# Kernel optimization log

Hardware: AMD Instinct MI355X
Metric: run time of the kernel (lower is better)

## Reference

```python
import jax, jax.numpy as jnp
import numpy as np

NC = 10          # num_clusters
D_MODEL = 512
H = 8
DK = 64          # d_model = H*DK
B = 8
L = 2048


def _mlp2(x, W1, b1, W2, b2):
    h = jax.nn.gelu(x @ W1 + b1, approximate=False)
    return h @ W2 + b2


def setup_inputs() -> dict:
    key = jax.random.key(0)
    ks = jax.random.split(key, 12)
    s_in = 1.0 / np.sqrt(D_MODEL)
    s_h = 1.0 / np.sqrt(4 * NC)
    s_nc = 1.0 / np.sqrt(NC)
    return {
        "Q": jax.random.normal(ks[0], (B, H, L, DK), jnp.float32),
        "K": jax.random.normal(ks[1], (B, H, L, DK), jnp.float32),
        "V": jax.random.normal(ks[2], (B, H, L, DK), jnp.float32),
        # cluster_k_proj: Linear(d_model,4*nc) GELU Linear(4*nc,nc); stored as [in,out]
        "Wk1": jax.random.normal(ks[3], (D_MODEL, 4 * NC), jnp.float32) * s_in,
        "bk1": jnp.zeros((4 * NC,), jnp.float32),
        "Wk2": jax.random.normal(ks[4], (4 * NC, NC), jnp.float32) * s_h,
        "bk2": jnp.zeros((NC,), jnp.float32),
        # cluster_q_proj
        "Wq1": jax.random.normal(ks[5], (D_MODEL, 4 * NC), jnp.float32) * s_in,
        "bq1": jnp.zeros((4 * NC,), jnp.float32),
        "Wq2": jax.random.normal(ks[6], (4 * NC, NC), jnp.float32) * s_h,
        "bq2": jnp.zeros((NC,), jnp.float32),
        # proj_back_to_cluster_k: Linear(nc, d_model) + GELU
        "Wp": jax.random.normal(ks[7], (NC, D_MODEL), jnp.float32) * s_nc,
        "bp": jnp.zeros((D_MODEL,), jnp.float32),
    }


def _forward(Q, K, V, Wk1, bk1, Wk2, bk2, Wq1, bq1, Wq2, bq2, Wp, bp):
    b, h, l, d_k = Q.shape
    nc = Wk2.shape[1]
    unfolding = 10 * nc

    def pool(x):
        # torch: MaxPool1d(kernel=9, stride=9(default), padding=4) on reshape(b, d_k*h, -1)
        x3 = x.reshape(b, d_k * h, -1)
        y = jax.lax.reduce_window(x3, -jnp.inf, jax.lax.max,
                                  (1, 1, 9), (1, 1, 9),
                                  ((0, 0), (0, 0), (4, 4)))
        return y.reshape(b, h, -1, d_k)

    Kp = pool(K)
    Vp = pool(V)
    l_k = Kp.shape[2]

    # pad along batch dim and take sliding windows of size `unfolding` (stride 1)
    pad = jnp.zeros((unfolding, h, l_k, d_k), Kp.dtype)
    K_padded = jnp.concatenate([pad, Kp[1:]], axis=0)      # [unfolding+b-1, h, l_k, d_k]
    idx = jnp.arange(b)[:, None] + jnp.arange(unfolding)[None, :]
    K_unf = K_padded[idx]                                  # [b, unfolding, h, l_k, d_k]
    K_unf = jnp.transpose(K_unf, (0, 2, 3, 4, 1))          # torch unfold puts window last
    K_unf = K_unf.reshape(b, l_k, unfolding, d_k * h)      # row-major reshape, as torch

    ck = jax.nn.softmax(_mlp2(K_unf, Wk1, bk1, Wk2, bk2), axis=-1)  # [b,l_k,u,nc]
    cq = jax.nn.softmax(_mlp2(K_unf, Wq1, bq1, Wq2, bq2), axis=-1)

    mu = jnp.mean(cq, axis=-1)                             # [b, l_k, unfolding]
    sigma = jax.nn.softplus(jnp.std(cq, axis=-1, ddof=1))  # torch std is unbiased
    x = jnp.mean(ck, axis=-1)
    log_prob = -0.5 * jnp.square((x - mu) / sigma) - jnp.log(sigma) - 0.5 * jnp.log(2.0 * jnp.pi)
    # torch CrossEntropyLoss(mu, mu): classes are dim 1 (l_k), soft prob targets
    logp = jax.nn.log_softmax(mu, axis=1)
    ce = jnp.mean(-jnp.sum(mu * logp, axis=1))
    loss = -jnp.mean(log_prob) + ce

    # fused scatter-style cluster centers: mean over window of cq with assigned cluster zeroed
    assign = jnp.argmax(cq, axis=-1)                       # [b, l_k, unfolding]
    onehot = jax.nn.one_hot(assign, nc, dtype=cq.dtype)    # [b, l_k, u, i] (constant wrt grad)
    total = jnp.sum(cq, axis=2)                            # [b, l_k, nc]
    S = jnp.einsum('blui,bluc->blic', onehot, cq)          # sum of cq at masked positions
    centers = (total[:, :, None, :] - S) / unfolding       # [b, l_k, nc_i, nc_c]
    centers = jnp.transpose(centers, (2, 0, 1, 3))         # [nc, b, l_k, nc]

    cc = jax.nn.gelu(centers @ Wp + bp, approximate=False) # [nc, b, l_k, d_model]
    cc = cc.reshape(b, h, nc, l_k, d_k)                    # faithful torch reshape

    scores = jnp.einsum('bhqd,bhckd->bhqk', Q, cc) / np.sqrt(d_k).astype(Q.dtype)
    attn = jax.nn.softmax(scores, axis=-1)
    context = jnp.einsum('bhqk,bhkd->bhqd', attn, Vp)
    return context, loss


def reference(Q, K, V, Wk1, bk1, Wk2, bk2, Wq1, bq1, Wq2, bq2, Wp, bp):
    return _forward(Q, K, V, Wk1, bk1, Wk2, bk2, Wq1, bq1, Wq2, bq2, Wp, bp)
```

## Files before the change

kernel.cpp:

```cpp
#include <hip/hip_runtime.h>
#include <math.h>

#define NCL 10
#define DM 512
#define NH 8
#define DK 64
#define NB 8
#define SL 2048
#define LK 228
#define UF 100
#define KP_PER_B (NH*LK*DK)
#define KP_TOT (NB*KP_PER_B)
#define NROWS (NB*LK*UF)
#define POOL_BLOCKS 7296

typedef __bf16 bf16_t;
typedef __attribute__((ext_vector_type(2))) __bf16 bf16x2;
typedef __attribute__((ext_vector_type(8))) __bf16 bf16x8;
typedef __attribute__((ext_vector_type(4))) float f32x4;

__device__ __forceinline__ float gelu_f(float x) {
    return 0.5f * x * (1.f + erff(x * 0.70710678118654752f));
}

__global__ void k_pool(const float* __restrict__ K, const float* __restrict__ V,
                       float* __restrict__ Kp, float* __restrict__ Vp,
                       const float* __restrict__ Wq1, bf16_t* __restrict__ W1b,
                       float* __restrict__ acc) {
    int bid = blockIdx.x;
    if (bid >= POOL_BLOCKS) {
        int i = (bid - POOL_BLOCKS) * 256 + threadIdx.x;
        if (i < 512 * 40) W1b[i] = (bf16_t)Wq1[i];
        if (bid == POOL_BLOCKS && threadIdx.x < 4) acc[threadIdx.x] = 0.f;
        return;
    }
    int idx = bid * 256 + threadIdx.x;
    const float* src = (idx < KP_TOT) ? K : V;
    float* dst = (idx < KP_TOT) ? Kp : Vp;
    int e = (idx < KP_TOT) ? idx : idx - KP_TOT;
    int b   = e / KP_PER_B;
    int off = e % KP_PER_B;
    int c  = off / LK;
    int pp = off % LK;
    int p0 = pp * 9 - 4;
    const float* base = src + (size_t)b * 1048576 + (size_t)c * 2048;
    float mx = -3.4e38f;
    #pragma unroll
    for (int j = 0; j < 9; ++j) {
        int p = p0 + j;
        if (p >= 0 && p < 2048) mx = fmaxf(mx, base[p]);
    }
    dst[e] = mx;
}

template<int B>
__device__ __forceinline__ void layer1(int tid, const bf16_t* __restrict__ W1b,
                                       const float* __restrict__ Sstf,
                                       float* __restrict__ hT) {
    #pragma unroll 1
    for (int k = 0; k < 2; ++k) {
        int vt = tid + (k << 8);
        if (vt < 500) {
            int m = vt / 5;
            int h8 = vt - m * 5;
            int bm = (12 * m) % 100;
            float h[8];
            #pragma unroll
            for (int i = 0; i < 8; ++i) h[i] = 0.f;
            #pragma unroll
            for (int s = 1; s <= B; ++s) {
                const int t = 99 - B + s;
                int d0 = t - bm; if (d0 < 0) d0 += 100;
                int r0 = ((m << 9) + d0 - t) / 100;
                const float* srow = &Sstf[s << 9];
                #pragma unroll
                for (int j = 0; j < 6; ++j) {
                    int c = d0 + j * 100;
                    if (j < 5 || c < 512) {
                        float v = srow[r0 + j];
                        bf16x8 w = *(const bf16x8*)&W1b[c * 40 + h8 * 8];
                        #pragma unroll
                        for (int i = 0; i < 8; ++i)
                            h[i] = fmaf(v, (float)w[i], h[i]);
                    }
                }
            }
            #pragma unroll
            for (int i = 0; i < 8; ++i) hT[m * 44 + h8 * 8 + i] = h[i];
        }
    }
}

__global__ __launch_bounds__(256, 4) void k_mlp(
        const float* __restrict__ Kp, const bf16_t* __restrict__ W1b,
        const float* __restrict__ bq1,
        const float* __restrict__ Wq2, const float* __restrict__ bq2,
        float* __restrict__ mu_g, float* __restrict__ centers_g,
        float* __restrict__ acc_g) {
    __shared__ __align__(16) char smem[34432];
    float* Sstf  = (float*)smem;
    float* hT    = (float*)(smem + 16384);
    float* stats = (float*)(smem + 33984);

    int tid = threadIdx.x;
    int bl = blockIdx.x;
    int b = bl / LK;
    int l = bl % LK;

    for (int s4 = tid; s4 < 128 * b; s4 += 256) {
        int bk = (s4 >> 7) + 1;
        int r4 = (s4 & 127) << 2;
        *(float4*)&Sstf[(bk << 9) + r4] =
            *(const float4*)&Kp[bk * KP_PER_B + l * 512 + r4];
    }
    if (tid < 111) stats[tid] = 0.f;
    if (b == 0) {
        for (int i = tid; i < 4400; i += 256) hT[i] = 0.f;
    }
    __syncthreads();

    switch (b) {
        case 1: layer1<1>(tid, W1b, Sstf, hT); break;
        case 2: layer1<2>(tid, W1b, Sstf, hT); break;
        case 3: layer1<3>(tid, W1b, Sstf, hT); break;
        case 4: layer1<4>(tid, W1b, Sstf, hT); break;
        case 5: layer1<5>(tid, W1b, Sstf, hT); break;
        case 6: layer1<6>(tid, W1b, Sstf, hT); break;
        case 7: layer1<7>(tid, W1b, Sstf, hT); break;
        default: break;
    }
    __syncthreads();

    for (int i = tid; i < 4000; i += 256) {
        int row = i / 40;
        int j = i - row * 40;
        hT[row * 44 + j] = gelu_f(hT[row * 44 + j] + bq1[j]);
    }
    __syncthreads();

    float* total_l = stats;
    float* S_l = stats + 10;
    float* lp_acc = stats + 110;

    if (tid < 100) {
        int row = tid;
        float g[40];
        #pragma unroll
        for (int j4 = 0; j4 < 10; ++j4) {
            float4 gv = *(const float4*)&hT[row * 44 + j4 * 4];
            g[j4 * 4 + 0] = gv.x; g[j4 * 4 + 1] = gv.y;
            g[j4 * 4 + 2] = gv.z; g[j4 * 4 + 3] = gv.w;
        }
        float out[10];
        #pragma unroll
        for (int c = 0; c < 10; ++c) out[c] = bq2[c];
        #pragma unroll
        for (int j = 0; j < 40; ++j) {
            float gj = g[j];
            #pragma unroll
            for (int c = 0; c < 10; ++c)
                out[c] = fmaf(gj, Wq2[j * 10 + c], out[c]);
        }
        float m = out[0]; int am = 0;
        #pragma unroll
        for (int c = 1; c < 10; ++c)
            if (out[c] > m) { m = out[c]; am = c; }
        float e[10], s = 0.f;
        #pragma unroll
        for (int c = 0; c < 10; ++c) { e[c] = expf(out[c] - m); s += e[c]; }
        float inv = 1.f / s;
        float cq[10], s1 = 0.f;
        #pragma unroll
        for (int c = 0; c < 10; ++c) { cq[c] = e[c] * inv; s1 += cq[c]; }
        float mean = s1 * 0.1f;
        float var = 0.f;
        #pragma unroll
        for (int c = 0; c < 10; ++c) { float d = cq[c] - mean; var += d * d; }
        float sd = sqrtf(var / 9.f);
        float sp = log1pf(expf(sd));
        float lp = -logf(sp) - 0.91893853320467274f;
        mu_g[bl * 100 + row] = mean;
        atomicAdd(lp_acc, lp);
        #pragma unroll
        for (int c = 0; c < 10; ++c) {
            atomicAdd(&total_l[c], cq[c]);
            atomicAdd(&S_l[am * 10 + c], cq[c]);
        }
    }
    __syncthreads();
    if (tid == 0) atomicAdd(&acc_g[0], lp_acc[0]);
    if (tid < 100) {
        centers_g[bl * 100 + tid] = (total_l[tid % 10] - S_l[tid]) * 0.01f;
    }
}

__global__ void k_ce(const float* __restrict__ mu_g, float* __restrict__ acc_g,
                     float* __restrict__ outp) {
    int bid = blockIdx.x;
    int b = bid / 100;
    int u = bid % 100;
    int lane = threadIdx.x;
    float v[4];
    #pragma unroll
    for (int t = 0; t < 4; ++t) {
        int l = lane + t * 64;
        v[t] = (l < LK) ? mu_g[(b * LK + l) * 100 + u] : -3.4e38f;
    }
    float m = fmaxf(fmaxf(v[0], v[1]), fmaxf(v[2], v[3]));
    for (int o = 32; o > 0; o >>= 1) m = fmaxf(m, __shfl_xor(m, o, 64));
    float se = 0.f;
    #pragma unroll
    for (int t = 0; t < 4; ++t) {
        int l = lane + t * 64;
        if (l < LK) se += expf(v[t] - m);
    }
    for (int o = 32; o > 0; o >>= 1) se += __shfl_xor(se, o, 64);
    float lse = m + logf(se);
    float dot = 0.f;
    #pragma unroll
    for (int t = 0; t < 4; ++t) {
        int l = lane + t * 64;
        if (l < LK) dot += v[t] * (v[t] - lse);
    }
    for (int o = 32; o > 0; o >>= 1) dot += __shfl_xor(dot, o, 64);
    if (lane == 0) {
        atomicAdd(&acc_g[1], -dot * (1.f / 800.f));
        __threadfence();
        unsigned int old = atomicAdd((unsigned int*)&acc_g[2], 1u);
        if (old == 799u) {
            __threadfence();
            outp[8388608] = -(acc_g[0] * (1.f / (float)NROWS)) + acc_g[1];
        }
    }
}

__global__ void k_ccs(const float* __restrict__ centers_g,
                      const float* __restrict__ Wp, const float* __restrict__ bp,
                      float* __restrict__ ccs) {
    int tid = blockIdx.x * 256 + threadIdx.x;
    if (tid >= KP_TOT) return;
    int k2d2 = tid % (LK * DK);
    int bh = tid / (LK * DK);
    float s = 0.f;
    #pragma unroll
    for (int i2 = 0; i2 < 10; ++i2) {
        int t2 = bh * 145920 + i2 * 14592 + k2d2;
        int i = t2 / 933888;
        int r1 = t2 % 933888;
        int bs = r1 / 116736;
        int r2 = r1 % 116736;
        int ls = r2 / 512;
        int mm = r2 % 512;
        const float* cen = centers_g + (bs * LK + ls) * 100 + i * 10;
        float val = bp[mm];
        #pragma unroll
        for (int c = 0; c < 10; ++c)
            val = fmaf(cen[c], Wp[c * 512 + mm], val);
        s += gelu_f(val);
    }
    ccs[tid] = s;
}

#define QT 128
__global__ __launch_bounds__(256, 3) void k_attn(
        const float* __restrict__ Q, const float* __restrict__ ccs,
        const float* __restrict__ Vp, float* __restrict__ outp) {
    __shared__ __align__(16) char smem[36864];
    bf16_t* Kl = (bf16_t*)(smem);
    bf16_t* Vt = (bf16_t*)(smem + 9216);
    bf16_t* Pl = (bf16_t*)(smem + 18432);

    int tid = threadIdx.x;
    int wid = tid >> 6;
    int lane = tid & 63;
    int ln = lane & 15;
    int qd = lane >> 4;
    int bid = blockIdx.x;
    int bh = bid >> 4;
    int qt = bid & 15;
    int qbase = qt * QT;

    const float* Qbh = Q + (size_t)bh * SL * DK;
    const float* Kbh = ccs + (size_t)bh * LK * DK;
    const float* Vbh = Vp + (size_t)bh * LK * DK;

    for (int s = tid; s < QT * 32; s += 256) {
        int r = s >> 5;
        int c2 = s & 31;
        float2 v = *(const float2*)&Qbh[(size_t)(qbase + r) * DK + c2 * 2];
        *(bf16x2*)&Pl[r * 72 + c2 * 2] = (bf16x2){(bf16_t)v.x, (bf16_t)v.y};
    }
    __syncthreads();
    bf16x8 qf[2][2];
    #pragma unroll
    for (int mt = 0; mt < 2; ++mt)
        #pragma unroll
        for (int ks = 0; ks < 2; ++ks)
            qf[mt][ks] = *(const bf16x8*)&Pl[(wid * 32 + mt * 16 + ln) * 72 + ks * 32 + qd * 8];

    f32x4 acc_o[2][4];
    float mrow[2][4], lrow[2][4];
    #pragma unroll
    for (int mt = 0; mt < 2; ++mt)
        #pragma unroll
        for (int t = 0; t < 4; ++t) {
            acc_o[mt][t] = (f32x4)(0.f);
            mrow[mt][t] = -3.0e38f;
            lrow[mt][t] = 0.f;
        }

    for (int ch = 0; ch < 4; ++ch) {
        int k0 = ch * 64;
        __syncthreads();
        for (int s = tid; s < 64 * 32; s += 256) {
            int kk = s >> 5;
            int c2 = s & 31;
            int key = k0 + kk;
            float2 v = (key < LK) ? *(const float2*)&Kbh[(size_t)key * DK + c2 * 2]
                                  : make_float2(0.f, 0.f);
            *(bf16x2*)&Kl[kk * 72 + c2 * 2] = (bf16x2){(bf16_t)v.x, (bf16_t)v.y};
        }
        for (int s = tid; s < 64 * 16; s += 256) {
            int kk = s >> 4;
            int c4 = s & 15;
            int key = k0 + kk;
            float4 v = (key < LK) ? *(const float4*)&Vbh[(size_t)key * DK + c4 * 4]
                                  : make_float4(0.f, 0.f, 0.f, 0.f);
            Vt[(c4 * 4 + 0) * 72 + kk] = (bf16_t)v.x;
            Vt[(c4 * 4 + 1) * 72 + kk] = (bf16_t)v.y;
            Vt[(c4 * 4 + 2) * 72 + kk] = (bf16_t)v.z;
            Vt[(c4 * 4 + 3) * 72 + kk] = (bf16_t)v.w;
        }
        __syncthreads();

        f32x4 accs[2][4];
        #pragma unroll
        for (int mt = 0; mt < 2; ++mt)
            #pragma unroll
            for (int nt = 0; nt < 4; ++nt) accs[mt][nt] = (f32x4)(0.f);
        #pragma unroll
        for (int ks = 0; ks < 2; ++ks) {
            #pragma unroll
            for (int nt = 0; nt < 4; ++nt) {
                bf16x8 bf = *(const bf16x8*)&Kl[(nt * 16 + ln) * 72 + ks * 32 + qd * 8];
                #pragma unroll
                for (int mt = 0; mt < 2; ++mt)
                    accs[mt][nt] = __builtin_amdgcn_mfma_f32_16x16x32_bf16(qf[mt][ks], bf, accs[mt][nt], 0, 0, 0);
            }
        }

        #pragma unroll
        for (int mt = 0; mt < 2; ++mt) {
            #pragma unroll
            for (int r = 0; r < 4; ++r) {
                float sv[4];
                #pragma unroll
                for (int nt = 0; nt < 4; ++nt) {
                    float s = accs[mt][nt][r] * 0.125f;
                    int key = k0 + nt * 16 + ln;
                    sv[nt] = (key < LK) ? s : -3.0e38f;
                }
                float rmax = fmaxf(fmaxf(sv[0], sv[1]), fmaxf(sv[2], sv[3]));
                #pragma unroll
                for (int o = 1; o < 16; o <<= 1)
                    rmax = fmaxf(rmax, __shfl_xor(rmax, o, 64));
                float mold = mrow[mt][r];
                float mnew = fmaxf(mold, rmax);
                float alpha = __expf(mold - mnew);
                float p[4], psum = 0.f;
                #pragma unroll
                for (int nt = 0; nt < 4; ++nt) {
                    p[nt] = __expf(sv[nt] - mnew);
                    psum += p[nt];
                }
                #pragma unroll
                for (int o = 1; o < 16; o <<= 1)
                    psum += __shfl_xor(psum, o, 64);
                lrow[mt][r] = lrow[mt][r] * alpha + psum;
                mrow[mt][r] = mnew;
                #pragma unroll
                for (int ntv = 0; ntv < 4; ++ntv)
                    acc_o[mt][ntv][r] *= alpha;
                int prow = (wid * 32 + mt * 16 + qd * 4 + r) * 72;
                #pragma unroll
                for (int nt = 0; nt < 4; ++nt)
                    Pl[prow + nt * 16 + ln] = (bf16_t)p[nt];
            }
        }

        #pragma unroll
        for (int ks = 0; ks < 2; ++ks) {
            bf16x8 pa[2];
            #pragma unroll
            for (int mt = 0; mt < 2; ++mt)
                pa[mt] = *(const bf16x8*)&Pl[(wid * 32 + mt * 16 + ln) * 72 + ks * 32 + qd * 8];
            #pragma unroll
            for (int ntv = 0; ntv < 4; ++ntv) {
                bf16x8 vb = *(const bf16x8*)&Vt[(ntv * 16 + ln) * 72 + ks * 32 + qd * 8];
                #pragma unroll
                for (int mt = 0; mt < 2; ++mt)
                    acc_o[mt][ntv] = __builtin_amdgcn_mfma_f32_16x16x32_bf16(pa[mt], vb, acc_o[mt][ntv], 0, 0, 0);
            }
        }
    }

    #pragma unroll
    for (int mt = 0; mt < 2; ++mt) {
        #pragma unroll
        for (int r = 0; r < 4; ++r) {
            float inv = 1.f / lrow[mt][r];
            int q_idx = qbase + wid * 32 + mt * 16 + qd * 4 + r;
            float* orow = outp + ((size_t)bh * SL + q_idx) * DK;
            #pragma unroll
            for (int ntv = 0; ntv < 4; ++ntv)
                orow[ntv * 16 + ln] = acc_o[mt][ntv][r] * inv;
        }
    }
}

extern "C" void kernel_launch(void* const* d_in, const int* in_sizes, int n_in,
                              void* d_out, int out_size, void* d_ws, size_t ws_size,
                              hipStream_t stream) {
    const float* Q   = (const float*)d_in[0];
    const float* K   = (const float*)d_in[1];
    const float* V   = (const float*)d_in[2];
    const float* Wq1 = (const float*)d_in[7];
    const float* bq1 = (const float*)d_in[8];
    const float* Wq2 = (const float*)d_in[9];
    const float* bq2 = (const float*)d_in[10];
    const float* Wp  = (const float*)d_in[11];
    const float* bp  = (const float*)d_in[12];
    float* out = (float*)d_out;

    float* ws      = (float*)d_ws;
    float* Kp      = ws;
    float* Vp      = ws + 933888;
    float* mu      = ws + 1867776;
    float* centers = ws + 2050176;
    float* ccs     = ws + 2232576;
    float* acc     = ws + 3166464;
    bf16_t* W1b    = (bf16_t*)(ws + 3166468);

    k_pool<<<POOL_BLOCKS + 80, 256, 0, stream>>>(K, V, Kp, Vp, Wq1, W1b, acc);
    k_mlp<<<NB * LK, 256, 0, stream>>>(Kp, W1b, bq1, Wq2, bq2, mu, centers, acc);
    k_ccs<<<(KP_TOT + 255) / 256, 256, 0, stream>>>(centers, Wp, bp, ccs);
    k_ce<<<NB * 100, 64, 0, stream>>>(mu, acc, out);
    k_attn<<<NB * NH * (SL / QT), 256, 0, stream>>>(Q, ccs, Vp, out);
}
```

Baseline: 349.8 us.

## Fuse GELU and second MLP layer into layer1, shrink shared memory

Folds the GELU and the second linear layer into the first-layer loop. Each thread's 8 hidden outputs are immediately multiplied by Wq2 and accumulated into a 100x10 shared buffer with atomics, so the 100x44 hidden staging buffer, one barrier and a separate GELU pass go away. Shared memory shrinks (Sstf drops its unused b=0 slot), launch bounds rise to 8 blocks per CU, and the block index is remapped so that consecutive blocks take different batches, which interleaves light and heavy work. The cost is shared-memory atomic contention (five threads per row) and extra register pressure from the fused epilogue.

```diff
diff --git a/kernel.cpp b/kernel.cpp
--- a/kernel.cpp
+++ b/kernel.cpp
@@ -56,7 +56,9 @@
 template<int B>
 __device__ __forceinline__ void layer1(int tid, const bf16_t* __restrict__ W1b,
                                        const float* __restrict__ Sstf,
-                                       float* __restrict__ hT) {
+                                       const float* __restrict__ bq1,
+                                       const float* __restrict__ Wq2,
+                                       float* __restrict__ pout) {
     #pragma unroll 1
     for (int k = 0; k < 2; ++k) {
         int vt = tid + (k << 8);
@@ -72,7 +74,7 @@
                 const int t = 99 - B + s;
                 int d0 = t - bm; if (d0 < 0) d0 += 100;
                 int r0 = ((m << 9) + d0 - t) / 100;
-                const float* srow = &Sstf[s << 9];
+                const float* srow = &Sstf[(s - 1) << 9];
                 #pragma unroll
                 for (int j = 0; j < 6; ++j) {
                     int c = d0 + j * 100;
@@ -85,56 +87,62 @@
                     }
                 }
             }
-            #pragma unroll
-            for (int i = 0; i < 8; ++i) hT[m * 44 + h8 * 8 + i] = h[i];
-        }
-    }
-}
-
-__global__ __launch_bounds__(256, 4) void k_mlp(
+            float po[10];
+            #pragma unroll
+            for (int c = 0; c < 10; ++c) po[c] = 0.f;
+            #pragma unroll
+            for (int i = 0; i < 8; ++i) {
+                float g = gelu_f(h[i] + bq1[h8 * 8 + i]);
+                const float* w2row = &Wq2[(h8 * 8 + i) * 10];
+                #pragma unroll
+                for (int c = 0; c < 10; ++c)
+                    po[c] = fmaf(g, w2row[c], po[c]);
+            }
+            #pragma unroll
+            for (int c = 0; c < 10; ++c)
+                atomicAdd(&pout[m * 10 + c], po[c]);
+        }
+    }
+}
+
+__global__ __launch_bounds__(256, 8) void k_mlp(
         const float* __restrict__ Kp, const bf16_t* __restrict__ W1b,
         const float* __restrict__ bq1,
         const float* __restrict__ Wq2, const float* __restrict__ bq2,
         float* __restrict__ mu_g, float* __restrict__ centers_g,
         float* __restrict__ acc_g) {
-    __shared__ __align__(16) char smem[34432];
+    __shared__ __align__(16) char smem[18784];
     float* Sstf  = (float*)smem;
-    float* hT    = (float*)(smem + 16384);
-    float* stats = (float*)(smem + 33984);
+    float* pout  = (float*)(smem + 14336);
+    float* stats = (float*)(smem + 18336);
 
     int tid = threadIdx.x;
-    int bl = blockIdx.x;
-    int b = bl / LK;
-    int l = bl % LK;
+    int bid = blockIdx.x;
+    int b = bid & 7;
+    int l = bid >> 3;
+    int bl = b * LK + l;
 
     for (int s4 = tid; s4 < 128 * b; s4 += 256) {
         int bk = (s4 >> 7) + 1;
         int r4 = (s4 & 127) << 2;
-        *(float4*)&Sstf[(bk << 9) + r4] =
+        *(float4*)&Sstf[((bk - 1) << 9) + r4] =
             *(const float4*)&Kp[bk * KP_PER_B + l * 512 + r4];
     }
+    if (b > 0) {
+        for (int i = tid; i < 1000; i += 256) pout[i] = 0.f;
+    }
     if (tid < 111) stats[tid] = 0.f;
-    if (b == 0) {
-        for (int i = tid; i < 4400; i += 256) hT[i] = 0.f;
-    }
     __syncthreads();
 
     switch (b) {
-        case 1: layer1<1>(tid, W1b, Sstf, hT); break;
-        case 2: layer1<2>(tid, W1b, Sstf, hT); break;
-        case 3: layer1<3>(tid, W1b, Sstf, hT); break;
-        case 4: layer1<4>(tid, W1b, Sstf, hT); break;
-        case 5: layer1<5>(tid, W1b, Sstf, hT); break;
-        case 6: layer1<6>(tid, W1b, Sstf, hT); break;
-        case 7: layer1<7>(tid, W1b, Sstf, hT); break;
+        case 1: layer1<1>(tid, W1b, Sstf, bq1, Wq2, pout); break;
+        case 2: layer1<2>(tid, W1b, Sstf, bq1, Wq2, pout); break;
+        case 3: layer1<3>(tid, W1b, Sstf, bq1, Wq2, pout); break;
+        case 4: layer1<4>(tid, W1b, Sstf, bq1, Wq2, pout); break;
+        case 5: layer1<5>(tid, W1b, Sstf, bq1, Wq2, pout); break;
+        case 6: layer1<6>(tid, W1b, Sstf, bq1, Wq2, pout); break;
+        case 7: layer1<7>(tid, W1b, Sstf, bq1, Wq2, pout); break;
         default: break;
-    }
-    __syncthreads();
-
-    for (int i = tid; i < 4000; i += 256) {
-        int row = i / 40;
-        int j = i - row * 40;
-        hT[row * 44 + j] = gelu_f(hT[row * 44 + j] + bq1[j]);
     }
     __syncthreads();
 
@@ -143,23 +151,19 @@
     float* lp_acc = stats + 110;
 
     if (tid < 100) {
-        int row = tid;
-        float g[40];
-        #pragma unroll
-        for (int j4 = 0; j4 < 10; ++j4) {
-            float4 gv = *(const float4*)&hT[row * 44 + j4 * 4];
-            g[j4 * 4 + 0] = gv.x; g[j4 * 4 + 1] = gv.y;
-            g[j4 * 4 + 2] = gv.z; g[j4 * 4 + 3] = gv.w;
-        }
         float out[10];
-        #pragma unroll
-        for (int c = 0; c < 10; ++c) out[c] = bq2[c];
-        #pragma unroll
-        for (int j = 0; j < 40; ++j) {
-            float gj = g[j];
-            #pragma unroll
-            for (int c = 0; c < 10; ++c)
-                out[c] = fmaf(gj, Wq2[j * 10 + c], out[c]);
+        if (b == 0) {
+            #pragma unroll
+            for (int c = 0; c < 10; ++c) out[c] = bq2[c];
+            for (int j = 0; j < 40; ++j) {
+                float g = gelu_f(bq1[j]);
+                #pragma unroll
+                for (int c = 0; c < 10; ++c)
+                    out[c] = fmaf(g, Wq2[j * 10 + c], out[c]);
+            }
+        } else {
+            #pragma unroll
+            for (int c = 0; c < 10; ++c) out[c] = pout[tid * 10 + c] + bq2[c];
         }
         float m = out[0]; int am = 0;
         #pragma unroll
@@ -179,7 +183,7 @@
         float sd = sqrtf(var / 9.f);
         float sp = log1pf(expf(sd));
         float lp = -logf(sp) - 0.91893853320467274f;
-        mu_g[bl * 100 + row] = mean;
+        mu_g[bl * 100 + tid] = mean;
         atomicAdd(lp_acc, lp);
         #pragma unroll
         for (int c = 0; c < 10; ++c) {
```

After: 425.2 us. 1.22x slower.
